# Optimization experiments

Hardware: AMD Instinct MI355X
Metric: run time of the kernel (lower is better)

Reference implementation:

```python
import jax, jax.numpy as jnp
import numpy as np

MASK_NUM = -2.0**32 + 1.0  # additive masking constant from the original layer


def setup_inputs() -> dict:
    key = jax.random.key(0)
    k1, k2, k3, k4 = jax.random.split(key, 4)
    BH, S, D = 32, 2048, 64  # batch*heads, seq_len, head_dim
    B = 4                    # original batch (masks are per-batch, tiled by heads)
    queries = jax.random.normal(k1, (BH, S, D), dtype=jnp.float32)
    keys_ = jax.random.normal(k2, (BH, S, D), dtype=jnp.float32)
    values = jax.random.normal(k3, (BH, S, D), dtype=jnp.float32)
    masks = jax.random.randint(k4, (B, S), 0, 2, dtype=jnp.int32)
    return {"queries": queries, "keys": keys_, "values": values, "masks": masks}


def reference(queries, keys, values, masks):
    BH, S, D = queries.shape
    # scores = Q K^T / sqrt(D)   -> [BH, S, S]
    scores = jnp.einsum("bqd,bkd->bqk", queries, keys) / (D ** 0.5)
    # key-padding mask: masks [B, S] tiled along axis 0 by BH // B, broadcast over query dim
    reps = BH // masks.shape[0]
    m = jnp.tile(masks.astype(jnp.float32), (reps, 1))[:, None, :]  # [BH, 1, S]
    scores = scores + m * MASK_NUM
    # causal (future) mask: keep lower triangle, replace rest with MASK_NUM
    tril = jnp.tril(jnp.ones((S, S), dtype=jnp.float32))
    scores = jnp.where(tril == 0, jnp.float32(MASK_NUM), scores)
    attn = jax.nn.softmax(scores, axis=-1)
    # dropout_rate = 0.0 -> identity
    return jnp.einsum("bqk,bkd->bqd", attn, values)
```

## Files before the change

### kernel.cpp

```cpp
#include <hip/hip_runtime.h>
#include <stdint.h>

#define S_LEN 2048
#define HDIM  64
#define NHEAD 32
#define NBATCH 4
#define QBLK 64
#define KBLK 64
#define QK_SCALE (0.125f * 1.44269504088896341f)
#define DEFER_THR 8.0f

typedef float f32x4 __attribute__((ext_vector_type(4)));
typedef short bf16x8 __attribute__((ext_vector_type(8)));

#define WS_MEANV 0
#define WS_MB    8192
#define WS_KBF   16384
#define KVBYTES  (NHEAD * 32 * 8192)
#define WS_VTBF  (WS_KBF + (size_t)KVBYTES)
#define WS_NEED_PRE (WS_VTBF + (size_t)KVBYTES)

static __device__ __forceinline__ unsigned int cvt_pk_bf16(float lo, float hi) {
    unsigned int r;
    asm("v_cvt_pk_bf16_f32 %0, %1, %2" : "=v"(r) : "v"(lo), "v"(hi));
    return r;
}

static __device__ __forceinline__ void load_lds16(const void* g, void* l) {
    __builtin_amdgcn_global_load_lds(
        (const __attribute__((address_space(1))) uint32_t*)g,
        (__attribute__((address_space(3))) uint32_t*)l, 16, 0, 0);
}

__global__ void maskprep_kernel(const int* __restrict__ masks,
                                unsigned long long* __restrict__ MB) {
    const int b = blockIdx.x;
    const int lane = threadIdx.x & 63;
    const int w = threadIdx.x >> 6;
    #pragma unroll
    for (int i = 0; i < 8; ++i) {
        const int word = i * 4 + w;
        const int m = masks[b * S_LEN + word * 64 + lane];
        const unsigned long long bits = __ballot(m != 0);
        if (lane == 0) MB[b * 32 + word] = bits;
    }
}

__global__ void meanv_atomic_kernel(const float* __restrict__ V, float* __restrict__ meanV) {
    const int bh = blockIdx.x >> 3, part = blockIdx.x & 7;
    const int t = threadIdx.x, d = t & 63, sub = t >> 6;
    const float* Vb = V + (size_t)bh * S_LEN * HDIM;
    float s = 0.f;
    const int k0 = part * 256 + sub * 64;
    for (int k = k0; k < k0 + 64; ++k) s += Vb[(size_t)k * HDIM + d];
    __shared__ float red[4][64];
    red[sub][d] = s;
    __syncthreads();
    if (t < 64) {
        float tot = red[0][t] + red[1][t] + red[2][t] + red[3][t];
        atomicAdd(&meanV[bh * HDIM + t], tot * (1.0f / (float)S_LEN));
    }
}

__global__ __launch_bounds__(256) void cvt_kernel(
    const float* __restrict__ K, const float* __restrict__ V,
    uint8_t* __restrict__ Kbf, uint8_t* __restrict__ Vtbf,
    float* __restrict__ meanV)
{
    const int bh = blockIdx.x >> 5, t = blockIdx.x & 31;
    const int tid = threadIdx.x, lane = tid & 63, w = tid >> 6;
    const size_t ho = (size_t)bh * S_LEN * HDIM;
    const size_t img = ((size_t)bh * 32 + t) * 8192;

    {
        const int kr = tid >> 2;
        const int kc = (tid & 3) << 4;
        const float4* kp = (const float4*)(K + ho + (size_t)(t * 64 + kr) * HDIM + kc);
        float4 a0 = kp[0], a1 = kp[1], a2 = kp[2], a3 = kp[3];
        int4 kv0, kv1;
        kv0.x = cvt_pk_bf16(a0.x, a0.y); kv0.y = cvt_pk_bf16(a0.z, a0.w);
        kv0.z = cvt_pk_bf16(a1.x, a1.y); kv0.w = cvt_pk_bf16(a1.z, a1.w);
        kv1.x = cvt_pk_bf16(a2.x, a2.y); kv1.y = cvt_pk_bf16(a2.z, a2.w);
        kv1.z = cvt_pk_bf16(a3.x, a3.y); kv1.w = cvt_pk_bf16(a3.z, a3.w);
        const int swz = (kr & 7) << 4;
        *(int4*)&Kbf[img + ((kr * 128 + kc * 2)      ^ swz)] = kv0;
        *(int4*)&Kbf[img + ((kr * 128 + kc * 2 + 16) ^ swz)] = kv1;
    }
    {
        const int vd = lane;
        const int vk = w * 16;
        const float* vp = V + ho + (size_t)(t * 64 + vk) * HDIM + vd;
        float va[16];
        float psum = 0.f;
        #pragma unroll
        for (int i = 0; i < 16; ++i) { va[i] = vp[(size_t)i * HDIM]; psum += va[i]; }
        int4 vv0, vv1;
        vv0.x = cvt_pk_bf16(va[0],  va[1]);  vv0.y = cvt_pk_bf16(va[2],  va[3]);
        vv0.z = cvt_pk_bf16(va[4],  va[5]);  vv0.w = cvt_pk_bf16(va[6],  va[7]);
        vv1.x = cvt_pk_bf16(va[8],  va[9]);  vv1.y = cvt_pk_bf16(va[10], va[11]);
        vv1.z = cvt_pk_bf16(va[12], va[13]); vv1.w = cvt_pk_bf16(va[14], va[15]);
        const int swz = (vd & 7) << 4;
        *(int4*)&Vtbf[img + ((vd * 128 + vk * 2)      ^ swz)] = vv0;
        *(int4*)&Vtbf[img + ((vd * 128 + vk * 2 + 16) ^ swz)] = vv1;
        __shared__ float red[4][64];
        red[w][vd] = psum;
        __syncthreads();
        if (tid < 64) {
            float tot = red[0][tid] + red[1][tid] + red[2][tid] + red[3][tid];
            atomicAdd(&meanV[bh * HDIM + tid], tot * (1.0f / (float)S_LEN));
        }
    }
}

#define P_OFF 32768
#define LDSB  40960

template<bool PRE>
__global__ __launch_bounds__(256) void attn_fwd(
    const float* __restrict__ Q, const float* __restrict__ K,
    const float* __restrict__ V, const float* __restrict__ meanV,
    const unsigned long long* __restrict__ MB,
    const uint8_t* __restrict__ Kbf, const uint8_t* __restrict__ Vtbf,
    float* __restrict__ out)
{
    __shared__ __align__(16) char lds[LDSB];
    const int tid  = threadIdx.x;
    const int lane = tid & 63;
    const int w    = tid >> 6;
    const int lq   = lane & 15;
    const int lk   = lane >> 4;

    const int bid  = blockIdx.x;
    const int nbid = (bid & 7) * 64 + (bid >> 3);
    const int bh   = nbid >> 4;
    const int j    = nbid & 15;
    const int b    = bh & (NBATCH - 1);

    const size_t ho = (size_t)bh * S_LEN * HDIM;
    const float* Qh = Q + ho;
    const float* Kh = K + ho;
    const float* Vh = V + ho;
    const uint8_t* kimg = Kbf  + (size_t)bh * 32 * 8192;
    const uint8_t* vimg = Vtbf + (size_t)bh * 32 * 8192;

    const int kr = tid >> 2;
    const int kc = (tid & 3) << 4;
    const int vd = lane;
    const int vk = w * 16;
    const float* Kp = Kh + (size_t)kr * HDIM + kc;
    const float* Vp = Vh + (size_t)vk * HDIM + vd;
    float4 ka0, ka1, ka2, ka3;
    float va[16];

    auto STAGE = [&](int t, int bufbase) {
        const uint8_t* gk = kimg + (size_t)t * 8192 + w * 2048 + lane * 16;
        const uint8_t* gv = vimg + (size_t)t * 8192 + w * 2048 + lane * 16;
        load_lds16(gk,        &lds[bufbase + w * 2048]);
        load_lds16(gk + 1024, &lds[bufbase + w * 2048 + 1024]);
        load_lds16(gv,        &lds[bufbase + 8192 + w * 2048]);
        load_lds16(gv + 1024, &lds[bufbase + 8192 + w * 2048 + 1024]);
    };
    auto LOADKV = [&](int kk0) {
        const float4* kp = (const float4*)(Kp + (size_t)kk0 * HDIM);
        ka0 = kp[0]; ka1 = kp[1]; ka2 = kp[2]; ka3 = kp[3];
        const float* vp = Vp + (size_t)kk0 * HDIM;
        #pragma unroll
        for (int i = 0; i < 16; ++i) va[i] = vp[(size_t)i * HDIM];
    };
    auto WRITEKV = [&](int bufbase) {
        int4 kv0, kv1;
        kv0.x = cvt_pk_bf16(ka0.x, ka0.y); kv0.y = cvt_pk_bf16(ka0.z, ka0.w);
        kv0.z = cvt_pk_bf16(ka1.x, ka1.y); kv0.w = cvt_pk_bf16(ka1.z, ka1.w);
        kv1.x = cvt_pk_bf16(ka2.x, ka2.y); kv1.y = cvt_pk_bf16(ka2.z, ka2.w);
        kv1.z = cvt_pk_bf16(ka3.x, ka3.y); kv1.w = cvt_pk_bf16(ka3.z, ka3.w);
        const int kswz = (kr & 7) << 4;
        *(int4*)&lds[bufbase + ((kr * 128 + kc * 2)      ^ kswz)] = kv0;
        *(int4*)&lds[bufbase + ((kr * 128 + kc * 2 + 16) ^ kswz)] = kv1;
        int4 vv0, vv1;
        vv0.x = cvt_pk_bf16(va[0],  va[1]);  vv0.y = cvt_pk_bf16(va[2],  va[3]);
        vv0.z = cvt_pk_bf16(va[4],  va[5]);  vv0.w = cvt_pk_bf16(va[6],  va[7]);
        vv1.x = cvt_pk_bf16(va[8],  va[9]);  vv1.y = cvt_pk_bf16(va[10], va[11]);
        vv1.z = cvt_pk_bf16(va[12], va[13]); vv1.w = cvt_pk_bf16(va[14], va[15]);
        const int vswz = (vd & 7) << 4;
        *(int4*)&lds[bufbase + 8192 + ((vd * 128 + vk * 2)      ^ vswz)] = vv0;
        *(int4*)&lds[bufbase + 8192 + ((vd * 128 + vk * 2 + 16) ^ vswz)] = vv1;
    };

    const int swz = (lq & 7) << 4;
    const int pbase = P_OFF + (w << 11);
    const int wq = w * 16 + lq;

    #pragma unroll 1
    for (int pass = 0; pass < 2; ++pass) {
        const int qb = pass ? (31 - j) : j;
        const int q0 = qb * QBLK;
        const int nt = qb + 1;

        bf16x8 qf[2];
        {
            const float* qrow = Qh + (size_t)(q0 + w * 16 + lq) * HDIM;
            #pragma unroll
            for (int c = 0; c < 2; ++c) {
                const int d0 = lk * 8 + c * 32;
                float4 f0 = *(const float4*)(qrow + d0);
                float4 f1 = *(const float4*)(qrow + d0 + 4);
                int4 qi;
                qi.x = cvt_pk_bf16(f0.x * QK_SCALE, f0.y * QK_SCALE);
                qi.y = cvt_pk_bf16(f0.z * QK_SCALE, f0.w * QK_SCALE);
                qi.z = cvt_pk_bf16(f1.x * QK_SCALE, f1.y * QK_SCALE);
                qi.w = cvt_pk_bf16(f1.z * QK_SCALE, f1.w * QK_SCALE);
                qf[c] = *(bf16x8*)&qi;
            }
        }

        f32x4 acc[4];
        #pragma unroll
        for (int g = 0; g < 4; ++g) acc[g] = (f32x4){0.f, 0.f, 0.f, 0.f};
        float m_r = -__builtin_inff();
        float l_r = 0.f;

        if constexpr (PRE) STAGE(0, 0);
        else { LOADKV(0); WRITEKV(0); }
        __syncthreads();

        for (int t = 0; t < nt; ++t) {
            const int cur = t & 1;
            const int kb  = cur << 14;
            const bool pre = (t + 1) < nt;
            if constexpr (PRE) { if (pre) STAGE(t + 1, (cur ^ 1) << 14); }
            else               { if (pre) LOADKV((t + 1) * KBLK); }

            f32x4 sacc[4];
            #pragma unroll
            for (int g = 0; g < 4; ++g) sacc[g] = (f32x4){0.f, 0.f, 0.f, 0.f};
            __builtin_amdgcn_s_setprio(1);
            #pragma unroll
            for (int c = 0; c < 2; ++c) {
                #pragma unroll
                for (int g = 0; g < 4; ++g) {
                    bf16x8 kf = *(const bf16x8*)&lds[kb + (((16 * g + lq) * 128 + 16 * lk + 64 * c) ^ swz)];
                    sacc[g] = __builtin_amdgcn_mfma_f32_16x16x32_bf16(kf, qf[c], sacc[g], 0, 0, 0);
                }
            }
            __builtin_amdgcn_s_setprio(0);

            const unsigned long long mb = MB[(b << 5) + t];
            const bool diag = (t == nt - 1);

            float mloc = sacc[0][0];
            #pragma unroll
            for (int g = 0; g < 4; ++g)
                #pragma unroll
                for (int r = 0; r < 4; ++r) mloc = fmaxf(mloc, sacc[g][r]);
            mloc = fmaxf(mloc, __shfl_xor(mloc, 16, 64));
            mloc = fmaxf(mloc, __shfl_xor(mloc, 32, 64));

            if (!__all(mloc - m_r <= DEFER_THR)) {
                const float newm = fmaxf(m_r, mloc);
                const float sc = exp2f(m_r - newm);
                l_r *= sc;
                m_r = newm;
                float scb[4];
                #pragma unroll
                for (int r = 0; r < 4; ++r) scb[r] = __shfl(sc, 4 * lk + r, 64);
                #pragma unroll
                for (int g = 0; g < 4; ++g)
                    #pragma unroll
                    for (int r = 0; r < 4; ++r) acc[g][r] *= scb[r];
            }

            float ls = 0.f;
            #pragma unroll
            for (int g = 0; g < 4; ++g) {
                const unsigned int nib = (unsigned int)(mb >> (16 * g + 4 * lk)) & 0xFu;
                #pragma unroll
                for (int r = 0; r < 4; ++r) {
                    const int kidx = 16 * g + 4 * lk + r;
                    float e = exp2f(sacc[g][r] - m_r);
                    const bool kill = ((nib >> r) & 1u) || (diag && kidx > wq);
                    e = kill ? 0.f : e;
                    sacc[g][r] = e;
                    ls += e;
                }
            }
            ls += __shfl_xor(ls, 16, 64);
            ls += __shfl_xor(ls, 32, 64);
            l_r += ls;

            #pragma unroll
            for (int g = 0; g < 4; ++g) {
                uint2 pw;
                pw.x = cvt_pk_bf16(sacc[g][0], sacc[g][1]);
                pw.y = cvt_pk_bf16(sacc[g][2], sacc[g][3]);
                *(uint2*)&lds[pbase + ((lq * 128 + 32 * g + 8 * lk) ^ swz)] = pw;
            }

            __builtin_amdgcn_s_setprio(1);
            #pragma unroll
            for (int c = 0; c < 2; ++c) {
                bf16x8 pa = *(const bf16x8*)&lds[pbase + ((lq * 128 + 16 * lk + 64 * c) ^ swz)];
                #pragma unroll
                for (int g = 0; g < 4; ++g) {
                    bf16x8 vb = *(const bf16x8*)&lds[kb + 8192 + (((lq + 16 * g) * 128 + 16 * lk + 64 * c) ^ swz)];
                    acc[g] = __builtin_amdgcn_mfma_f32_16x16x32_bf16(pa, vb, acc[g], 0, 0, 0);
                }
            }
            __builtin_amdgcn_s_setprio(0);

            if constexpr (!PRE) { if (pre) WRITEKV((cur ^ 1) << 14); }
            __syncthreads();
        }

        float lr_b[4];
        #pragma unroll
        for (int r = 0; r < 4; ++r) lr_b[r] = __shfl(l_r, 4 * lk + r, 64);
        #pragma unroll
        for (int r = 0; r < 4; ++r) {
            const int qrow = q0 + w * 16 + 4 * lk + r;
            float* orow = out + ho + (size_t)qrow * HDIM;
            if (lr_b[r] == 0.f) {
                #pragma unroll
                for (int g = 0; g < 4; ++g) orow[lq + 16 * g] = meanV[bh * HDIM + lq + 16 * g];
            } else {
                const float inv = 1.0f / lr_b[r];
                #pragma unroll
                for (int g = 0; g < 4; ++g) orow[lq + 16 * g] = acc[g][r] * inv;
            }
        }
    }
}

extern "C" void kernel_launch(void* const* d_in, const int* in_sizes, int n_in,
                              void* d_out, int out_size, void* d_ws, size_t ws_size,
                              hipStream_t stream)
{
    const float* Q     = (const float*)d_in[0];
    const float* K     = (const float*)d_in[1];
    const float* V     = (const float*)d_in[2];
    const int*   masks = (const int*)d_in[3];
    float* out = (float*)d_out;

    char* ws = (char*)d_ws;
    float* meanV = (float*)(ws + WS_MEANV);
    unsigned long long* MB = (unsigned long long*)(ws + WS_MB);

    hipMemsetAsync(meanV, 0, NHEAD * HDIM * sizeof(float), stream);
    maskprep_kernel<<<dim3(NBATCH), dim3(256), 0, stream>>>(masks, MB);

    if (ws_size >= WS_NEED_PRE) {
        uint8_t* Kbf  = (uint8_t*)(ws + WS_KBF);
        uint8_t* Vtbf = (uint8_t*)(ws + WS_VTBF);
        cvt_kernel<<<dim3(NHEAD * 32), dim3(256), 0, stream>>>(K, V, Kbf, Vtbf, meanV);
        attn_fwd<true><<<dim3(512), dim3(256), 0, stream>>>(Q, K, V, meanV, MB, Kbf, Vtbf, out);
    } else {
        meanv_atomic_kernel<<<dim3(256), dim3(256), 0, stream>>>(V, meanV);
        attn_fwd<false><<<dim3(512), dim3(256), 0, stream>>>(Q, K, V, meanV, MB, nullptr, nullptr, out);
    }
}
```

Baseline: 155.5 us.

## Use 128-key tiles in attention, fuse mask/mean prep into convert kernel

The attention loop now processes 128 keys per iteration (two 64-key images), with double-buffered LDS grown to 80KB of dynamic shared memory. The upper half is skipped on even diagonal blocks. Masking moves to before the max, as large negative scores. Mask bit-packing and per-tile V partial means are folded into the convert kernel, which removes the memset, atomics, the mask kernel and the fp32 fallback path. The aim is fewer loop iterations and barriers per block and fewer launches, at the cost of LDS occupancy and a slower fully-masked-row fallback that sums 32 partials.

```diff
diff --git a/kernel.cpp b/kernel.cpp
--- a/kernel.cpp
+++ b/kernel.cpp
@@ -5,71 +5,45 @@
 #define HDIM  64
 #define NHEAD 32
 #define NBATCH 4
-#define QBLK 64
-#define KBLK 64
 #define QK_SCALE (0.125f * 1.44269504088896341f)
 #define DEFER_THR 8.0f
+#define NEG_BIG (-1e30f)
 
 typedef float f32x4 __attribute__((ext_vector_type(4)));
 typedef short bf16x8 __attribute__((ext_vector_type(8)));
 
-#define WS_MEANV 0
-#define WS_MB    8192
-#define WS_KBF   16384
-#define KVBYTES  (NHEAD * 32 * 8192)
-#define WS_VTBF  (WS_KBF + (size_t)KVBYTES)
-#define WS_NEED_PRE (WS_VTBF + (size_t)KVBYTES)
+#define WS_MB    0
+#define WS_MVP   1024
+#define WS_KBF   132096
+#define KVB      (NHEAD * 32 * 8192)
+#define WS_VTBF  (WS_KBF + (size_t)KVB)
 
 static __device__ __forceinline__ unsigned int cvt_pk_bf16(float lo, float hi) {
     unsigned int r;
     asm("v_cvt_pk_bf16_f32 %0, %1, %2" : "=v"(r) : "v"(lo), "v"(hi));
     return r;
 }
-
+static __device__ __forceinline__ float bf2f(unsigned short u) {
+    return __uint_as_float((unsigned int)u << 16);
+}
 static __device__ __forceinline__ void load_lds16(const void* g, void* l) {
     __builtin_amdgcn_global_load_lds(
         (const __attribute__((address_space(1))) uint32_t*)g,
         (__attribute__((address_space(3))) uint32_t*)l, 16, 0, 0);
 }
 
-__global__ void maskprep_kernel(const int* __restrict__ masks,
-                                unsigned long long* __restrict__ MB) {
-    const int b = blockIdx.x;
-    const int lane = threadIdx.x & 63;
-    const int w = threadIdx.x >> 6;
-    #pragma unroll
-    for (int i = 0; i < 8; ++i) {
-        const int word = i * 4 + w;
-        const int m = masks[b * S_LEN + word * 64 + lane];
-        const unsigned long long bits = __ballot(m != 0);
-        if (lane == 0) MB[b * 32 + word] = bits;
-    }
-}
-
-__global__ void meanv_atomic_kernel(const float* __restrict__ V, float* __restrict__ meanV) {
-    const int bh = blockIdx.x >> 3, part = blockIdx.x & 7;
-    const int t = threadIdx.x, d = t & 63, sub = t >> 6;
-    const float* Vb = V + (size_t)bh * S_LEN * HDIM;
-    float s = 0.f;
-    const int k0 = part * 256 + sub * 64;
-    for (int k = k0; k < k0 + 64; ++k) s += Vb[(size_t)k * HDIM + d];
-    __shared__ float red[4][64];
-    red[sub][d] = s;
-    __syncthreads();
-    if (t < 64) {
-        float tot = red[0][t] + red[1][t] + red[2][t] + red[3][t];
-        atomicAdd(&meanV[bh * HDIM + t], tot * (1.0f / (float)S_LEN));
-    }
-}
-
 __global__ __launch_bounds__(256) void cvt_kernel(
     const float* __restrict__ K, const float* __restrict__ V,
+    const int* __restrict__ masks,
     uint8_t* __restrict__ Kbf, uint8_t* __restrict__ Vtbf,
-    float* __restrict__ meanV)
+    unsigned short* __restrict__ mvp, unsigned long long* __restrict__ MB)
 {
-    const int bh = blockIdx.x >> 5, t = blockIdx.x & 31;
+    const int bid = blockIdx.x;
+    const int xcd = bid & 7, rem = bid >> 3;
+    const int bh  = xcd * 4 + (rem >> 5);
+    const int t   = rem & 31;
     const int tid = threadIdx.x, lane = tid & 63, w = tid >> 6;
-    const size_t ho = (size_t)bh * S_LEN * HDIM;
+    const size_t ho  = (size_t)bh * S_LEN * HDIM;
     const size_t img = ((size_t)bh * 32 + t) * 8192;
 
     {
@@ -107,23 +81,24 @@
         __syncthreads();
         if (tid < 64) {
             float tot = red[0][tid] + red[1][tid] + red[2][tid] + red[3][tid];
-            atomicAdd(&meanV[bh * HDIM + tid], tot * (1.0f / (float)S_LEN));
+            mvp[(bh * 32 + t) * 64 + tid] = (unsigned short)(cvt_pk_bf16(tot * (1.0f / (float)S_LEN), 0.f) & 0xFFFF);
         }
     }
-}
-
-#define P_OFF 32768
-#define LDSB  40960
-
-template<bool PRE>
+    if (bh < NBATCH && tid < 64) {
+        const int m = masks[bh * S_LEN + t * 64 + lane];
+        const unsigned long long bits = __ballot(m != 0);
+        if (lane == 0) MB[bh * 32 + t] = bits;
+    }
+}
+
 __global__ __launch_bounds__(256) void attn_fwd(
-    const float* __restrict__ Q, const float* __restrict__ K,
-    const float* __restrict__ V, const float* __restrict__ meanV,
+    const float* __restrict__ Q,
+    const unsigned short* __restrict__ mvp,
     const unsigned long long* __restrict__ MB,
     const uint8_t* __restrict__ Kbf, const uint8_t* __restrict__ Vtbf,
     float* __restrict__ out)
 {
-    __shared__ __align__(16) char lds[LDSB];
+    extern __shared__ __align__(16) char lds[];
     const int tid  = threadIdx.x;
     const int lane = tid & 63;
     const int w    = tid >> 6;
@@ -138,63 +113,37 @@
 
     const size_t ho = (size_t)bh * S_LEN * HDIM;
     const float* Qh = Q + ho;
-    const float* Kh = K + ho;
-    const float* Vh = V + ho;
     const uint8_t* kimg = Kbf  + (size_t)bh * 32 * 8192;
     const uint8_t* vimg = Vtbf + (size_t)bh * 32 * 8192;
 
-    const int kr = tid >> 2;
-    const int kc = (tid & 3) << 4;
-    const int vd = lane;
-    const int vk = w * 16;
-    const float* Kp = Kh + (size_t)kr * HDIM + kc;
-    const float* Vp = Vh + (size_t)vk * HDIM + vd;
-    float4 ka0, ka1, ka2, ka3;
-    float va[16];
-
-    auto STAGE = [&](int t, int bufbase) {
-        const uint8_t* gk = kimg + (size_t)t * 8192 + w * 2048 + lane * 16;
-        const uint8_t* gv = vimg + (size_t)t * 8192 + w * 2048 + lane * 16;
-        load_lds16(gk,        &lds[bufbase + w * 2048]);
-        load_lds16(gk + 1024, &lds[bufbase + w * 2048 + 1024]);
-        load_lds16(gv,        &lds[bufbase + 8192 + w * 2048]);
-        load_lds16(gv + 1024, &lds[bufbase + 8192 + w * 2048 + 1024]);
+    auto STAGE = [&](int img0, bool two, int bufb) {
+        const uint8_t* gk = kimg + (size_t)img0 * 8192 + w * 2048 + lane * 16;
+        const uint8_t* gv = vimg + (size_t)img0 * 8192 + w * 2048 + lane * 16;
+        char* lk0 = &lds[bufb + w * 2048];
+        char* lv0 = &lds[bufb + 16384 + w * 2048];
+        load_lds16(gk,        lk0);
+        load_lds16(gk + 1024, lk0 + 1024);
+        load_lds16(gv,        lv0);
+        load_lds16(gv + 1024, lv0 + 1024);
+        if (two) {
+            load_lds16(gk + 8192, lk0 + 8192);
+            load_lds16(gk + 9216, lk0 + 9216);
+            load_lds16(gv + 8192, lv0 + 8192);
+            load_lds16(gv + 9216, lv0 + 9216);
+        }
     };
-    auto LOADKV = [&](int kk0) {
-        const float4* kp = (const float4*)(Kp + (size_t)kk0 * HDIM);
-        ka0 = kp[0]; ka1 = kp[1]; ka2 = kp[2]; ka3 = kp[3];
-        const float* vp = Vp + (size_t)kk0 * HDIM;
-        #pragma unroll
-        for (int i = 0; i < 16; ++i) va[i] = vp[(size_t)i * HDIM];
-    };
-    auto WRITEKV = [&](int bufbase) {
-        int4 kv0, kv1;
-        kv0.x = cvt_pk_bf16(ka0.x, ka0.y); kv0.y = cvt_pk_bf16(ka0.z, ka0.w);
-        kv0.z = cvt_pk_bf16(ka1.x, ka1.y); kv0.w = cvt_pk_bf16(ka1.z, ka1.w);
-        kv1.x = cvt_pk_bf16(ka2.x, ka2.y); kv1.y = cvt_pk_bf16(ka2.z, ka2.w);
-        kv1.z = cvt_pk_bf16(ka3.x, ka3.y); kv1.w = cvt_pk_bf16(ka3.z, ka3.w);
-        const int kswz = (kr & 7) << 4;
-        *(int4*)&lds[bufbase + ((kr * 128 + kc * 2)      ^ kswz)] = kv0;
-        *(int4*)&lds[bufbase + ((kr * 128 + kc * 2 + 16) ^ kswz)] = kv1;
-        int4 vv0, vv1;
-        vv0.x = cvt_pk_bf16(va[0],  va[1]);  vv0.y = cvt_pk_bf16(va[2],  va[3]);
-        vv0.z = cvt_pk_bf16(va[4],  va[5]);  vv0.w = cvt_pk_bf16(va[6],  va[7]);
-        vv1.x = cvt_pk_bf16(va[8],  va[9]);  vv1.y = cvt_pk_bf16(va[10], va[11]);
-        vv1.z = cvt_pk_bf16(va[12], va[13]); vv1.w = cvt_pk_bf16(va[14], va[15]);
-        const int vswz = (vd & 7) << 4;
-        *(int4*)&lds[bufbase + 8192 + ((vd * 128 + vk * 2)      ^ vswz)] = vv0;
-        *(int4*)&lds[bufbase + 8192 + ((vd * 128 + vk * 2 + 16) ^ vswz)] = vv1;
-    };
-
-    const int swz = (lq & 7) << 4;
-    const int pbase = P_OFF + (w << 11);
-    const int wq = w * 16 + lq;
+
+    const int swz   = (lq & 7) << 4;
+    const int pswz  = (lq & 15) << 4;
+    const int pbase = 65536 + (w << 12);
+    const int prow  = lq << 8;
 
     #pragma unroll 1
     for (int pass = 0; pass < 2; ++pass) {
         const int qb = pass ? (31 - j) : j;
-        const int q0 = qb * QBLK;
-        const int nt = qb + 1;
+        const int q0 = qb * 64;
+        const int nt = (qb >> 1) + 1;
+        const int wqa = q0 + w * 16 + lq;
 
         bf16x8 qf[2];
         {
@@ -216,42 +165,67 @@
         f32x4 acc[4];
         #pragma unroll
         for (int g = 0; g < 4; ++g) acc[g] = (f32x4){0.f, 0.f, 0.f, 0.f};
-        float m_r = -__builtin_inff();
+        float m_r = 0.f;
         float l_r = 0.f;
 
-        if constexpr (PRE) STAGE(0, 0);
-        else { LOADKV(0); WRITEKV(0); }
+        STAGE(0, qb >= 1, 0);
         __syncthreads();
 
-        for (int t = 0; t < nt; ++t) {
-            const int cur = t & 1;
-            const int kb  = cur << 14;
-            const bool pre = (t + 1) < nt;
-            if constexpr (PRE) { if (pre) STAGE(t + 1, (cur ^ 1) << 14); }
-            else               { if (pre) LOADKV((t + 1) * KBLK); }
-
-            f32x4 sacc[4];
-            #pragma unroll
-            for (int g = 0; g < 4; ++g) sacc[g] = (f32x4){0.f, 0.f, 0.f, 0.f};
+        for (int it = 0; it < nt; ++it) {
+            const int kb     = (it & 1) << 15;
+            const bool diag  = (it == nt - 1);
+            const bool skipHi = diag && ((qb & 1) == 0);
+            if (!diag) {
+                const int a = 2 * it + 2;
+                STAGE(a, (a + 1) <= qb, kb ^ 32768);
+            }
+
+            f32x4 sacc[8];
+            #pragma unroll
+            for (int g = 0; g < 8; ++g) sacc[g] = (f32x4){0.f, 0.f, 0.f, 0.f};
             __builtin_amdgcn_s_setprio(1);
             #pragma unroll
             for (int c = 0; c < 2; ++c) {
                 #pragma unroll
                 for (int g = 0; g < 4; ++g) {
-                    bf16x8 kf = *(const bf16x8*)&lds[kb + (((16 * g + lq) * 128 + 16 * lk + 64 * c) ^ swz)];
+                    bf16x8 kf = *(const bf16x8*)&lds[kb + ((16 * g + lq) * 128 + ((16 * lk + 64 * c) ^ swz))];
                     sacc[g] = __builtin_amdgcn_mfma_f32_16x16x32_bf16(kf, qf[c], sacc[g], 0, 0, 0);
                 }
             }
+            if (!skipHi) {
+                #pragma unroll
+                for (int c = 0; c < 2; ++c) {
+                    #pragma unroll
+                    for (int g = 4; g < 8; ++g) {
+                        bf16x8 kf = *(const bf16x8*)&lds[kb + 8192 + ((16 * (g - 4) + lq) * 128 + ((16 * lk + 64 * c) ^ swz))];
+                        sacc[g] = __builtin_amdgcn_mfma_f32_16x16x32_bf16(kf, qf[c], sacc[g], 0, 0, 0);
+                    }
+                }
+            }
             __builtin_amdgcn_s_setprio(0);
 
-            const unsigned long long mb = MB[(b << 5) + t];
-            const bool diag = (t == nt - 1);
-
-            float mloc = sacc[0][0];
-            #pragma unroll
-            for (int g = 0; g < 4; ++g)
-                #pragma unroll
-                for (int r = 0; r < 4; ++r) mloc = fmaxf(mloc, sacc[g][r]);
+            if (diag) {
+                const int wqrel = wqa - it * 128;
+                #pragma unroll
+                for (int g = 0; g < 8; ++g)
+                    #pragma unroll
+                    for (int r = 0; r < 4; ++r)
+                        if (16 * g + 4 * lk + r > wqrel) sacc[g][r] = NEG_BIG;
+            }
+            const unsigned long long mb0 = MB[(b << 5) + 2 * it];
+            const unsigned long long mb1 = MB[(b << 5) + 2 * it + 1];
+            float mloc = NEG_BIG;
+            #pragma unroll
+            for (int g = 0; g < 8; ++g) {
+                const unsigned long long mbw = (g < 4) ? mb0 : mb1;
+                const unsigned int nib = (unsigned int)(mbw >> (16 * (g & 3) + 4 * lk)) & 0xFu;
+                #pragma unroll
+                for (int r = 0; r < 4; ++r) {
+                    float s = ((nib >> r) & 1u) ? NEG_BIG : sacc[g][r];
+                    sacc[g][r] = s;
+                    mloc = fmaxf(mloc, s);
+                }
+            }
             mloc = fmaxf(mloc, __shfl_xor(mloc, 16, 64));
             mloc = fmaxf(mloc, __shfl_xor(mloc, 32, 64));
 
@@ -269,20 +243,17 @@
                     for (int r = 0; r < 4; ++r) acc[g][r] *= scb[r];
             }
 
-            float ls = 0.f;
-            #pragma unroll
-            for (int g = 0; g < 4; ++g) {
-                const unsigned int nib = (unsigned int)(mb >> (16 * g + 4 * lk)) & 0xFu;
+            float ls0 = 0.f, ls1 = 0.f;
+            #pragma unroll
+            for (int g = 0; g < 8; ++g) {
                 #pragma unroll
                 for (int r = 0; r < 4; ++r) {
-                    const int kidx = 16 * g + 4 * lk + r;
                     float e = exp2f(sacc[g][r] - m_r);
-                    const bool kill = ((nib >> r) & 1u) || (diag && kidx > wq);
-                    e = kill ? 0.f : e;
                     sacc[g][r] = e;
-                    ls += e;
-                }
-            }
+                    if (g & 1) ls1 += e; else ls0 += e;
+                }
+            }
+            float ls = ls0 + ls1;
             ls += __shfl_xor(ls, 16, 64);
             ls += __shfl_xor(ls, 32, 64);
             l_r += ls;
@@ -292,22 +263,41 @@
                 uint2 pw;
                 pw.x = cvt_pk_bf16(sacc[g][0], sacc[g][1]);
                 pw.y = cvt_pk_bf16(sacc[g][2], sacc[g][3]);
-                *(uint2*)&lds[pbase + ((lq * 128 + 32 * g + 8 * lk) ^ swz)] = pw;
+                *(uint2*)&lds[pbase + prow + (((32 * g + 8 * lk)) ^ pswz)] = pw;
+            }
+            if (!skipHi) {
+                #pragma unroll
+                for (int g = 4; g < 8; ++g) {
+                    uint2 pw;
+                    pw.x = cvt_pk_bf16(sacc[g][0], sacc[g][1]);
+                    pw.y = cvt_pk_bf16(sacc[g][2], sacc[g][3]);
+                    *(uint2*)&lds[pbase + prow + (((32 * g + 8 * lk)) ^ pswz)] = pw;
+                }
             }
 
             __builtin_amdgcn_s_setprio(1);
             #pragma unroll
             for (int c = 0; c < 2; ++c) {
-                bf16x8 pa = *(const bf16x8*)&lds[pbase + ((lq * 128 + 16 * lk + 64 * c) ^ swz)];
+                bf16x8 pa = *(const bf16x8*)&lds[pbase + prow + ((64 * c + 16 * lk) ^ pswz)];
                 #pragma unroll
                 for (int g = 0; g < 4; ++g) {
-                    bf16x8 vb = *(const bf16x8*)&lds[kb + 8192 + (((lq + 16 * g) * 128 + 16 * lk + 64 * c) ^ swz)];
+                    bf16x8 vb = *(const bf16x8*)&lds[kb + 16384 + ((lq + 16 * g) * 128 + ((16 * lk + 64 * c) ^ swz))];
                     acc[g] = __builtin_amdgcn_mfma_f32_16x16x32_bf16(pa, vb, acc[g], 0, 0, 0);
                 }
             }
+            if (!skipHi) {
+                #pragma unroll
+                for (int c = 2; c < 4; ++c) {
+                    bf16x8 pa = *(const bf16x8*)&lds[pbase + prow + ((64 * c + 16 * lk) ^ pswz)];
+                    #pragma unroll
+                    for (int g = 0; g < 4; ++g) {
+                        bf16x8 vb = *(const bf16x8*)&lds[kb + 16384 + 8192 + ((lq + 16 * g) * 128 + ((16 * lk + 64 * (c - 2)) ^ swz))];
+                        acc[g] = __builtin_amdgcn_mfma_f32_16x16x32_bf16(pa, vb, acc[g], 0, 0, 0);
+                    }
+                }
+            }
             __builtin_amdgcn_s_setprio(0);
 
-            if constexpr (!PRE) { if (pre) WRITEKV((cur ^ 1) << 14); }
             __syncthreads();
         }
 
@@ -320,7 +310,12 @@
             float* orow = out + ho + (size_t)qrow * HDIM;
             if (lr_b[r] == 0.f) {
                 #pragma unroll
-                for (int g = 0; g < 4; ++g) orow[lq + 16 * g] = meanV[bh * HDIM + lq + 16 * g];
+                for (int g = 0; g < 4; ++g) {
+                    float s = 0.f;
+                    for (int tt = 0; tt < 32; ++tt)
+                        s += bf2f(mvp[(bh * 32 + tt) * 64 + lq + 16 * g]);
+                    orow[lq + 16 * g] = s;
+                }
             } else {
                 const float inv = 1.0f / lr_b[r];
                 #pragma unroll
@@ -341,19 +336,14 @@
     float* out = (float*)d_out;
 
     char* ws = (char*)d_ws;
-    float* meanV = (float*)(ws + WS_MEANV);
     unsigned long long* MB = (unsigned long long*)(ws + WS_MB);
-
-    hipMemsetAsync(meanV, 0, NHEAD * HDIM * sizeof(float), stream);
-    maskprep_kernel<<<dim3(NBATCH), dim3(256), 0, stream>>>(masks, MB);
-
-    if (ws_size >= WS_NEED_PRE) {
-        uint8_t* Kbf  = (uint8_t*)(ws + WS_KBF);
-        uint8_t* Vtbf = (uint8_t*)(ws + WS_VTBF);
-        cvt_kernel<<<dim3(NHEAD * 32), dim3(256), 0, stream>>>(K, V, Kbf, Vtbf, meanV);
-        attn_fwd<true><<<dim3(512), dim3(256), 0, stream>>>(Q, K, V, meanV, MB, Kbf, Vtbf, out);
-    } else {
-        meanv_atomic_kernel<<<dim3(256), dim3(256), 0, stream>>>(V, meanV);
-        attn_fwd<false><<<dim3(512), dim3(256), 0, stream>>>(Q, K, V, meanV, MB, nullptr, nullptr, out);
-    }
-}
+    unsigned short* mvp    = (unsigned short*)(ws + WS_MVP);
+    uint8_t* Kbf  = (uint8_t*)(ws + WS_KBF);
+    uint8_t* Vtbf = (uint8_t*)(ws + WS_VTBF);
+
+    hipFuncSetAttribute(reinterpret_cast<const void*>(&attn_fwd),
+                        hipFuncAttributeMaxDynamicSharedMemorySize, 81920);
+
+    cvt_kernel<<<dim3(1024), dim3(256), 0, stream>>>(K, V, masks, Kbf, Vtbf, mvp, MB);
+    attn_fwd<<<dim3(512), dim3(256), 81920, stream>>>(Q, mvp, MB, Kbf, Vtbf, out);
+}
```

Result: faster. 145.8 us (-6.3%).
